# Optimization experiments

Measured on AMD Instinct MI355X. Metric: run time of the kernel, lower is better.

The kernel has to match this reference:

```python
import jax, jax.numpy as jnp
import numpy as np

S, B, D, H = 2048, 2, 1024, 16
DK = D // H


def _rope_tables(seq_len, dk):
    inv_freq = 1.0 / (10000.0 ** (np.arange(0, dk, 2, dtype=np.float32) / dk))
    ang = np.arange(seq_len, dtype=np.float32)[:, None] * inv_freq[None, :]  # [S, dk/2]
    ang = np.concatenate([ang, ang], axis=-1)  # [S, dk]
    cos = jnp.asarray(np.cos(ang))[None, None]  # [1,1,S,dk]
    sin = jnp.asarray(np.sin(ang))[None, None]
    return cos, sin


def rotate_half(x):
    x1, x2 = x[..., : x.shape[-1] // 2], x[..., x.shape[-1] // 2 :]
    return jnp.concatenate([-x2, x1], axis=-1)


def apply_rope(x, cos, sin):
    return x * cos + rotate_half(x) * sin


def setup_inputs() -> dict:
    key = jax.random.key(0)
    ks = jax.random.split(key, 12)
    Q = jax.random.normal(ks[0], (S, B, D), dtype=jnp.float32)
    K = jax.random.normal(ks[1], (S, B, D), dtype=jnp.float32)
    V = jax.random.normal(ks[2], (S, B, D), dtype=jnp.float32)
    s = 0.02
    W_q = jax.random.normal(ks[3], (D, D), dtype=jnp.float32) * s
    W_k = jax.random.normal(ks[4], (D, D), dtype=jnp.float32) * s
    W_v = jax.random.normal(ks[5], (D, D), dtype=jnp.float32) * s
    W_o = jax.random.normal(ks[6], (D, D), dtype=jnp.float32) * s
    b_q = jnp.zeros((D,), jnp.float32)
    b_k = jnp.zeros((D,), jnp.float32)
    b_v = jnp.zeros((D,), jnp.float32)
    b_o = jnp.zeros((D,), jnp.float32)
    cos, sin = _rope_tables(S, DK)
    mask = jnp.triu(jnp.ones((S, S), dtype=bool), k=1)[None, None]  # causal, True = masked
    return {
        "Q": Q, "K": K, "V": V,
        "W_q": W_q, "b_q": b_q, "W_k": W_k, "b_k": b_k,
        "W_v": W_v, "b_v": b_v, "W_o": W_o, "b_o": b_o,
        "q_rotary_cos": cos, "q_rotary_sin": sin,
        "k_rotary_cos": cos, "k_rotary_sin": sin,
        "mask": mask,
    }


def reference(Q, K, V, W_q, b_q, W_k, b_k, W_v, b_v, W_o, b_o,
              q_rotary_cos, q_rotary_sin, k_rotary_cos, k_rotary_sin, mask):
    q_len, bsz, _ = Q.shape
    # [S,B,D] -> [S,B,H,dk] -> [B,H,S,dk]
    def proj(x, W, b):
        y = x @ W.T + b
        return y.reshape(x.shape[0], bsz, H, DK).transpose(1, 2, 0, 3)
    q_s = apply_rope(proj(Q, W_q, b_q), q_rotary_cos, q_rotary_sin)
    k_s = apply_rope(proj(K, W_k, b_k), k_rotary_cos, k_rotary_sin)
    v_s = proj(V, W_v, b_v)
    scores = jnp.einsum("bhqd,bhkd->bhqk", q_s, k_s) / jnp.sqrt(jnp.float32(DK))
    scores = jnp.where(mask, jnp.float32(-1e9), scores)
    attn = jax.nn.softmax(scores, axis=-1)
    context = jnp.einsum("bhqk,bhkd->bhqd", attn, v_s)  # [B,H,S,dk]
    context = context.transpose(2, 0, 1, 3).reshape(q_len, bsz, D)
    return context @ W_o.T + b_o
```

## Files before the change

### kernel.cpp

```cpp
#include <hip/hip_runtime.h>
#include <cstdint>
#include <cstddef>

typedef __bf16 bf16;
typedef __bf16 bf16x2 __attribute__((ext_vector_type(2)));
typedef __bf16 bf16x4 __attribute__((ext_vector_type(4)));
typedef __bf16 bf16x8 __attribute__((ext_vector_type(8)));
typedef float f32x4 __attribute__((ext_vector_type(4)));

#define S_LEN 2048
#define BATCH 2
#define DM 1024
#define NH 16
#define DKH 64
#define MTOT (S_LEN * BATCH)

__device__ __forceinline__ void gload_lds16(const void* g, void* l) {
    __builtin_amdgcn_global_load_lds((const __attribute__((address_space(1))) uint32_t*)g,
                                     (__attribute__((address_space(3))) uint32_t*)l, 16, 0, 0);
}

__device__ __forceinline__ uint32_t pack2(float a, float b) {
    bf16x2 v; v[0] = (bf16)a; v[1] = (bf16)b;
    return __builtin_bit_cast(uint32_t, v);
}

struct ConvArgs { const float* src[7]; bf16* dst[7]; };

__global__ __launch_bounds__(256) void convert_all(ConvArgs a) {
    int gid = blockIdx.x * 256 + threadIdx.x;
    int tid, off;
    if (gid < 3 * 524288) { tid = gid >> 19; off = gid & 524287; }
    else { int r = gid - 3 * 524288; tid = 3 + (r >> 17); off = r & 131071; }
    const float4* s4 = (const float4*)a.src[tid];
    float4 x = s4[2 * off], y = s4[2 * off + 1];
    bf16x8 v;
    v[0] = (bf16)x.x; v[1] = (bf16)x.y; v[2] = (bf16)x.z; v[3] = (bf16)x.w;
    v[4] = (bf16)y.x; v[5] = (bf16)y.y; v[6] = (bf16)y.z; v[7] = (bf16)y.w;
    *(bf16x8*)(a.dst[tid] + 8 * (size_t)off) = v;
}

__device__ __forceinline__ void gemm_core(const bf16* __restrict__ A, const bf16* __restrict__ Bt,
                                          const float* __restrict__ bias, void* __restrict__ out,
                                          int mode, bf16* As, bf16* Bs) {
    const int K = DM;
    int t = threadIdx.x;
    int lane = t & 63, wave = t >> 6;
    int lm = lane & 15, quad = lane >> 4;
    int m0 = blockIdx.y * 128, n0 = blockIdx.x * 128;
    int wm = (wave >> 1) * 64, wn = (wave & 1) * 64;
    f32x4 acc[4][4] = {};
    int g0 = t, g1 = t + 256;
    const bf16* agp0 = A + (size_t)(m0 + (g0 >> 2)) * K + (g0 & 3) * 8;
    const bf16* agp1 = A + (size_t)(m0 + (g1 >> 2)) * K + (g1 & 3) * 8;
    const bf16* bgp0 = Bt + (size_t)(n0 + (g0 >> 2)) * K + (g0 & 3) * 8;
    const bf16* bgp1 = Bt + (size_t)(n0 + (g1 >> 2)) * K + (g1 & 3) * 8;
    bf16* al0 = As + wave * 512;
    bf16* al1 = As + 2048 + wave * 512;
    bf16* bl0 = Bs + wave * 512;
    bf16* bl1 = Bs + 2048 + wave * 512;
    for (int k0 = 0; k0 < K; k0 += 32) {
        gload_lds16(agp0 + k0, al0);
        gload_lds16(agp1 + k0, al1);
        gload_lds16(bgp0 + k0, bl0);
        gload_lds16(bgp1 + k0, bl1);
        __syncthreads();
        bf16x8 af[4], bfr[4];
#pragma unroll
        for (int i = 0; i < 4; ++i)
            af[i] = *(const bf16x8*)(As + (wm + i * 16 + lm) * 32 + quad * 8);
#pragma unroll
        for (int j = 0; j < 4; ++j)
            bfr[j] = *(const bf16x8*)(Bs + (wn + j * 16 + lm) * 32 + quad * 8);
#pragma unroll
        for (int i = 0; i < 4; ++i)
#pragma unroll
            for (int j = 0; j < 4; ++j)
                acc[i][j] = __builtin_amdgcn_mfma_f32_16x16x32_bf16(af[i], bfr[j], acc[i][j], 0, 0, 0);
        __syncthreads();
    }
#pragma unroll
    for (int i = 0; i < 4; ++i) {
#pragma unroll
        for (int j = 0; j < 4; ++j) {
            int col = n0 + wn + j * 16 + lm;
            float bv = bias[col];
            f32x4 v = acc[i][j];
#pragma unroll
            for (int r = 0; r < 4; ++r) {
                int row = m0 + wm + i * 16 + quad * 4 + r;
                float val = v[r] + bv;
                if (mode == 0) {
                    ((bf16*)out)[(size_t)row * DM + col] = (bf16)val;
                } else if (mode == 1) {
                    int s = row >> 1, b = row & 1;
                    int h = col >> 6, dk = col & 63;
                    ((bf16*)out)[((size_t)(b * NH + h) * DKH + dk) * S_LEN + s] = (bf16)val;
                } else {
                    ((float*)out)[(size_t)row * DM + col] = val;
                }
            }
        }
    }
}

struct QKVArgs { const bf16* A[3]; const bf16* W[3]; const float* bias[3]; void* out[3]; int mode[3]; };

__global__ __launch_bounds__(256) void gemm_qkv(QKVArgs args) {
    __shared__ __align__(16) bf16 As[128 * 32];
    __shared__ __align__(16) bf16 Bs[128 * 32];
    int z = blockIdx.z;
    gemm_core(args.A[z], args.W[z], args.bias[z], args.out[z], args.mode[z], As, Bs);
}

__global__ __launch_bounds__(256) void gemm_one(const bf16* __restrict__ A, const bf16* __restrict__ Bt,
                                                const float* __restrict__ bias, void* __restrict__ out,
                                                int mode) {
    __shared__ __align__(16) bf16 As[128 * 32];
    __shared__ __align__(16) bf16 Bs[128 * 32];
    gemm_core(A, Bt, bias, out, mode, As, Bs);
}

__global__ __launch_bounds__(256) void rope_kernel(bf16* __restrict__ q, bf16* __restrict__ k,
                                                   const float* __restrict__ qc, const float* __restrict__ qs,
                                                   const float* __restrict__ kc, const float* __restrict__ ks) {
    int i = blockIdx.x * 256 + threadIdx.x;
    int dk = i & 31;
    int h = (i >> 5) & 15;
    int b = (i >> 9) & 1;
    int s = i >> 10;
    size_t base = ((size_t)s * BATCH + b) * DM + h * DKH;
    int ti = s * DKH + dk;
    const float qscale = 0.125f * 1.44269504088896f;
    float c1 = qc[ti], s1 = qs[ti], c2 = qc[ti + 32], s2 = qs[ti + 32];
    float x1 = (float)q[base + dk], x2 = (float)q[base + dk + 32];
    q[base + dk]      = (bf16)((x1 * c1 - x2 * s1) * qscale);
    q[base + dk + 32] = (bf16)((x2 * c2 + x1 * s2) * qscale);
    float kc1 = kc[ti], ks1 = ks[ti], kc2 = kc[ti + 32], ks2 = ks[ti + 32];
    float y1 = (float)k[base + dk], y2 = (float)k[base + dk + 32];
    k[base + dk]      = (bf16)(y1 * kc1 - y2 * ks1);
    k[base + dk + 32] = (bf16)(y2 * kc2 + y1 * ks2);
}

__global__ __launch_bounds__(256, 2) void flash_kernel(const bf16* __restrict__ qp, const bf16* __restrict__ kp,
                                                       const bf16* __restrict__ vT, bf16* __restrict__ ctx) {
    int qt = 15 - blockIdx.x;
    int bh = blockIdx.y;
    int b = bh >> 4, h = bh & 15;
    int t = threadIdx.x, lane = t & 63, wave = t >> 6;
    int lm = lane & 15, quad = lane >> 4;
    __shared__ __align__(16) bf16 Ks[2 * 64 * 32];
    __shared__ __align__(16) bf16 Vs[2 * 64 * 32];
    __shared__ __align__(16) uint32_t Pb[4][16 * 36];
    uint32_t* pw = &Pb[wave][0];
    const int q0w = qt * 128 + wave * 32;

    bf16x8 aq[2][2];
#pragma unroll
    for (int u = 0; u < 2; ++u) {
        const bf16* qrow = qp + ((size_t)(q0w + u * 16 + lm) * BATCH + b) * DM + h * DKH;
        aq[u][0] = *(const bf16x8*)(qrow + quad * 8);
        aq[u][1] = *(const bf16x8*)(qrow + 32 + quad * 8);
    }
    f32x4 o[2][4] = {};
    float m_u[2] = {-1e30f, -1e30f};
    float l_u[2] = {0.f, 0.f};

    int gA = t, gB = t + 256;
    int aKv = (gA & 255) >> 2, aDq = ((gA >> 8) << 2) + (gA & 3);
    int bKv = (gB & 255) >> 2, bDq = ((gB >> 8) << 2) + (gB & 3);
    const bf16* kgp0 = kp + ((size_t)aKv * BATCH + b) * DM + h * DKH + aDq * 8;
    const bf16* kgp1 = kp + ((size_t)bKv * BATCH + b) * DM + h * DKH + bDq * 8;
    const bf16* vgp0 = vT + ((size_t)bh * DKH + aKv) * S_LEN + aDq * 8;
    const bf16* vgp1 = vT + ((size_t)bh * DKH + bKv) * S_LEN + bDq * 8;
    bf16* kl0 = Ks + wave * 512;
    bf16* kl1 = Ks + 2048 + wave * 512;
    bf16* vl0 = Vs + wave * 512;
    bf16* vl1 = Vs + 2048 + wave * 512;

    const int kv_end = qt * 128 + 128;
    const int wave_qmax = q0w + 31;
    const size_t kstep = (size_t)BATCH * DM;

    for (int kv0 = 0; kv0 < kv_end; kv0 += 64) {
        gload_lds16(kgp0 + (size_t)kv0 * kstep, kl0);
        gload_lds16(kgp1 + (size_t)kv0 * kstep, kl1);
        gload_lds16(vgp0 + kv0, vl0);
        gload_lds16(vgp1 + kv0, vl1);
        __syncthreads();
        if (kv0 <= wave_qmax) {
            bf16x8 kf[4][2], vf[4][2];
#pragma unroll
            for (int nt = 0; nt < 4; ++nt) {
                kf[nt][0] = *(const bf16x8*)(Ks + (nt * 16 + lm) * 32 + quad * 8);
                kf[nt][1] = *(const bf16x8*)(Ks + 2048 + (nt * 16 + lm) * 32 + quad * 8);
            }
#pragma unroll
            for (int dt = 0; dt < 4; ++dt) {
                vf[dt][0] = *(const bf16x8*)(Vs + (dt * 16 + lm) * 32 + quad * 8);
                vf[dt][1] = *(const bf16x8*)(Vs + 2048 + (dt * 16 + lm) * 32 + quad * 8);
            }
            const f32x4 zero = {0.f, 0.f, 0.f, 0.f};
            f32x4 sc[2][4];
#pragma unroll
            for (int u = 0; u < 2; ++u)
#pragma unroll
                for (int nt = 0; nt < 4; ++nt) {
                    sc[u][nt] = __builtin_amdgcn_mfma_f32_16x16x32_bf16(kf[nt][0], aq[u][0], zero, 0, 0, 0);
                    sc[u][nt] = __builtin_amdgcn_mfma_f32_16x16x32_bf16(kf[nt][1], aq[u][1], sc[u][nt], 0, 0, 0);
                }
#pragma unroll
            for (int u = 0; u < 2; ++u) {
                int qu0 = q0w + u * 16;
                if (kv0 + 63 > qu0) {
#pragma unroll
                    for (int nt = 0; nt < 4; ++nt)
#pragma unroll
                        for (int r = 0; r < 4; ++r) {
                            int kvg = kv0 + nt * 16 + quad * 4 + r;
                            if (kvg > qu0 + lm) sc[u][nt][r] = -1e30f;
                        }
                }
            }
#pragma unroll
            for (int u = 0; u < 2; ++u) {
                float mx = sc[u][0][0];
#pragma unroll
                for (int nt = 0; nt < 4; ++nt)
#pragma unroll
                    for (int r = 0; r < 4; ++r) mx = fmaxf(mx, sc[u][nt][r]);
                mx = fmaxf(mx, __shfl_xor(mx, 16, 64));
                mx = fmaxf(mx, __shfl_xor(mx, 32, 64));
                float mn = fmaxf(m_u[u], mx);
                float al = exp2f(m_u[u] - mn);
                m_u[u] = mn;
                float rs = 0.f;
                uint32_t pk[8];
#pragma unroll
                for (int nt = 0; nt < 4; ++nt)
#pragma unroll
                    for (int rp = 0; rp < 2; ++rp) {
                        float p0 = exp2f(sc[u][nt][2 * rp] - mn);
                        float p1 = exp2f(sc[u][nt][2 * rp + 1] - mn);
                        rs += p0 + p1;
                        pk[nt * 2 + rp] = pack2(p0, p1);
                    }
                rs += __shfl_xor(rs, 16, 64);
                rs += __shfl_xor(rs, 32, 64);
                l_u[u] = l_u[u] * al + rs;
#pragma unroll
                for (int dt = 0; dt < 4; ++dt) o[u][dt] *= al;
#pragma unroll
                for (int nt = 0; nt < 4; ++nt)
#pragma unroll
                    for (int rp = 0; rp < 2; ++rp)
                        pw[lm * 36 + nt * 8 + quad * 2 + rp] = pk[nt * 2 + rp];
                __builtin_amdgcn_wave_barrier();
                const uint32_t* pr = pw + lm * 36;
                bf16x8 pf0 = *(const bf16x8*)(pr + quad * 4);
                bf16x8 pf1 = *(const bf16x8*)(pr + 16 + quad * 4);
#pragma unroll
                for (int dt = 0; dt < 4; ++dt) {
                    o[u][dt] = __builtin_amdgcn_mfma_f32_16x16x32_bf16(vf[dt][0], pf0, o[u][dt], 0, 0, 0);
                    o[u][dt] = __builtin_amdgcn_mfma_f32_16x16x32_bf16(vf[dt][1], pf1, o[u][dt], 0, 0, 0);
                }
                __builtin_amdgcn_wave_barrier();
            }
        }
        __syncthreads();
    }
#pragma unroll
    for (int u = 0; u < 2; ++u) {
        float linv = 1.f / l_u[u];
        int qg = q0w + u * 16 + lm;
        bf16* crow = ctx + ((size_t)qg * BATCH + b) * DM + h * DKH;
#pragma unroll
        for (int dt = 0; dt < 4; ++dt) {
            bf16x4 v;
#pragma unroll
            for (int r = 0; r < 4; ++r) v[r] = (bf16)(o[u][dt][r] * linv);
            *(bf16x4*)(crow + dt * 16 + quad * 4) = v;
        }
    }
}

extern "C" void kernel_launch(void* const* d_in, const int* in_sizes, int n_in,
                              void* d_out, int out_size, void* d_ws, size_t ws_size,
                              hipStream_t stream) {
    const float* Q    = (const float*)d_in[0];
    const float* K    = (const float*)d_in[1];
    const float* V    = (const float*)d_in[2];
    const float* Wq   = (const float*)d_in[3];
    const float* bq   = (const float*)d_in[4];
    const float* Wk   = (const float*)d_in[5];
    const float* bk   = (const float*)d_in[6];
    const float* Wv   = (const float*)d_in[7];
    const float* bv   = (const float*)d_in[8];
    const float* Wo   = (const float*)d_in[9];
    const float* bo   = (const float*)d_in[10];
    const float* qcos = (const float*)d_in[11];
    const float* qsin = (const float*)d_in[12];
    const float* kcos = (const float*)d_in[13];
    const float* ksin = (const float*)d_in[14];

    char* ws = (char*)d_ws;
    const size_t SZ_ACT = (size_t)MTOT * DM * sizeof(bf16);
    const size_t SZ_W   = (size_t)DM * DM * sizeof(bf16);
    bf16* qb  = (bf16*)ws; ws += SZ_ACT;
    bf16* kb  = (bf16*)ws; ws += SZ_ACT;
    bf16* vb  = (bf16*)ws; ws += SZ_ACT;
    bf16* wqb = (bf16*)ws; ws += SZ_W;
    bf16* wkb = (bf16*)ws; ws += SZ_W;
    bf16* wvb = (bf16*)ws; ws += SZ_W;
    bf16* wob = (bf16*)ws; ws += SZ_W;
    bf16* qpr = (bf16*)ws; ws += SZ_ACT;
    bf16* kpr = (bf16*)ws; ws += SZ_ACT;
    bf16* vTp = (bf16*)ws; ws += SZ_ACT;
    bf16* ctx = (bf16*)ws; ws += SZ_ACT;

    ConvArgs ca;
    ca.src[0] = Q;  ca.dst[0] = qb;
    ca.src[1] = K;  ca.dst[1] = kb;
    ca.src[2] = V;  ca.dst[2] = vb;
    ca.src[3] = Wq; ca.dst[3] = wqb;
    ca.src[4] = Wk; ca.dst[4] = wkb;
    ca.src[5] = Wv; ca.dst[5] = wvb;
    ca.src[6] = Wo; ca.dst[6] = wob;
    convert_all<<<8192, 256, 0, stream>>>(ca);

    QKVArgs qa;
    qa.A[0] = qb; qa.W[0] = wqb; qa.bias[0] = bq; qa.out[0] = qpr; qa.mode[0] = 0;
    qa.A[1] = kb; qa.W[1] = wkb; qa.bias[1] = bk; qa.out[1] = kpr; qa.mode[1] = 0;
    qa.A[2] = vb; qa.W[2] = wvb; qa.bias[2] = bv; qa.out[2] = vTp; qa.mode[2] = 1;
    gemm_qkv<<<dim3(DM / 128, MTOT / 128, 3), 256, 0, stream>>>(qa);

    rope_kernel<<<(S_LEN * BATCH * NH * 32) / 256, 256, 0, stream>>>(qpr, kpr, qcos, qsin, kcos, ksin);

    flash_kernel<<<dim3(S_LEN / 128, BATCH * NH), 256, 0, stream>>>(qpr, kpr, vTp, ctx);

    gemm_one<<<dim3(DM / 128, MTOT / 128), 256, 0, stream>>>(ctx, wob, bo, (float*)d_out, 2);
}
```

Baseline: 301.4 us.

## Fuse RoPE into QKV GEMM epilogue and restructure flash attention tiling

Applies the rotary embedding and the softmax scale inside the Q/K projection GEMM epilogue. It pairs each column with its partner accumulator (j^2, a 32-column offset within the 64-wide head), which removes the separate rope kernel and its extra read/write pass. The flash kernel changes to 64-query tiles with one 16-row strip per wave, 32 blocks per head and launch bounds of 3. K/V staging changes from direct global-to-LDS loads to register-prefetched double buffering with padded LDS rows (72 elements). This trades more grid parallelism and overlap for less reuse of each K/V tile across query rows.

```diff
diff --git a/kernel.cpp b/kernel.cpp
--- a/kernel.cpp
+++ b/kernel.cpp
@@ -42,7 +42,8 @@
 
 __device__ __forceinline__ void gemm_core(const bf16* __restrict__ A, const bf16* __restrict__ Bt,
                                           const float* __restrict__ bias, void* __restrict__ out,
-                                          int mode, bf16* As, bf16* Bs) {
+                                          int mode, const float* __restrict__ cosp,
+                                          const float* __restrict__ sinp, bf16* As, bf16* Bs) {
     const int K = DM;
     int t = threadIdx.x;
     int lane = t & 63, wave = t >> 6;
@@ -80,207 +81,202 @@
         __syncthreads();
     }
 #pragma unroll
+    for (int j = 0; j < 4; ++j) {
+        float bcol = bias[n0 + wn + j * 16 + lm];
+#pragma unroll
+        for (int i = 0; i < 4; ++i)
+#pragma unroll
+            for (int r = 0; r < 4; ++r) acc[i][j][r] += bcol;
+    }
+#pragma unroll
     for (int i = 0; i < 4; ++i) {
 #pragma unroll
         for (int j = 0; j < 4; ++j) {
             int col = n0 + wn + j * 16 + lm;
-            float bv = bias[col];
-            f32x4 v = acc[i][j];
 #pragma unroll
             for (int r = 0; r < 4; ++r) {
                 int row = m0 + wm + i * 16 + quad * 4 + r;
-                float val = v[r] + bv;
-                if (mode == 0) {
-                    ((bf16*)out)[(size_t)row * DM + col] = (bf16)val;
-                } else if (mode == 1) {
+                float val = acc[i][j][r];
+                if (mode == 1) {
                     int s = row >> 1, b = row & 1;
                     int h = col >> 6, dk = col & 63;
                     ((bf16*)out)[((size_t)(b * NH + h) * DKH + dk) * S_LEN + s] = (bf16)val;
+                } else if (mode == 2) {
+                    ((float*)out)[(size_t)row * DM + col] = val;
                 } else {
-                    ((float*)out)[(size_t)row * DM + col] = val;
+                    int s = row >> 1, dk = col & 63;
+                    float c = cosp[s * 64 + dk], sn = sinp[s * 64 + dk];
+                    float partner = acc[i][j ^ 2][r];
+                    float v2 = val * c + (dk < 32 ? -partner : partner) * sn;
+                    if (mode == 3) v2 *= 0.125f * 1.44269504088896f;
+                    ((bf16*)out)[(size_t)row * DM + col] = (bf16)v2;
                 }
             }
         }
     }
 }
 
-struct QKVArgs { const bf16* A[3]; const bf16* W[3]; const float* bias[3]; void* out[3]; int mode[3]; };
+struct QKVArgs {
+    const bf16* A[3]; const bf16* W[3]; const float* bias[3];
+    void* out[3]; const float* cs[3]; const float* sn[3]; int mode[3];
+};
 
 __global__ __launch_bounds__(256) void gemm_qkv(QKVArgs args) {
     __shared__ __align__(16) bf16 As[128 * 32];
     __shared__ __align__(16) bf16 Bs[128 * 32];
     int z = blockIdx.z;
-    gemm_core(args.A[z], args.W[z], args.bias[z], args.out[z], args.mode[z], As, Bs);
+    gemm_core(args.A[z], args.W[z], args.bias[z], args.out[z], args.mode[z],
+              args.cs[z], args.sn[z], As, Bs);
 }
 
 __global__ __launch_bounds__(256) void gemm_one(const bf16* __restrict__ A, const bf16* __restrict__ Bt,
-                                                const float* __restrict__ bias, void* __restrict__ out,
-                                                int mode) {
+                                                const float* __restrict__ bias, void* __restrict__ out) {
     __shared__ __align__(16) bf16 As[128 * 32];
     __shared__ __align__(16) bf16 Bs[128 * 32];
-    gemm_core(A, Bt, bias, out, mode, As, Bs);
-}
-
-__global__ __launch_bounds__(256) void rope_kernel(bf16* __restrict__ q, bf16* __restrict__ k,
-                                                   const float* __restrict__ qc, const float* __restrict__ qs,
-                                                   const float* __restrict__ kc, const float* __restrict__ ks) {
-    int i = blockIdx.x * 256 + threadIdx.x;
-    int dk = i & 31;
-    int h = (i >> 5) & 15;
-    int b = (i >> 9) & 1;
-    int s = i >> 10;
-    size_t base = ((size_t)s * BATCH + b) * DM + h * DKH;
-    int ti = s * DKH + dk;
-    const float qscale = 0.125f * 1.44269504088896f;
-    float c1 = qc[ti], s1 = qs[ti], c2 = qc[ti + 32], s2 = qs[ti + 32];
-    float x1 = (float)q[base + dk], x2 = (float)q[base + dk + 32];
-    q[base + dk]      = (bf16)((x1 * c1 - x2 * s1) * qscale);
-    q[base + dk + 32] = (bf16)((x2 * c2 + x1 * s2) * qscale);
-    float kc1 = kc[ti], ks1 = ks[ti], kc2 = kc[ti + 32], ks2 = ks[ti + 32];
-    float y1 = (float)k[base + dk], y2 = (float)k[base + dk + 32];
-    k[base + dk]      = (bf16)(y1 * kc1 - y2 * ks1);
-    k[base + dk + 32] = (bf16)(y2 * kc2 + y1 * ks2);
-}
-
-__global__ __launch_bounds__(256, 2) void flash_kernel(const bf16* __restrict__ qp, const bf16* __restrict__ kp,
+    gemm_core(A, Bt, bias, out, 2, nullptr, nullptr, As, Bs);
+}
+
+#define LROW 72
+#define LBUF (64 * LROW)
+
+__global__ __launch_bounds__(256, 3) void flash_kernel(const bf16* __restrict__ qp, const bf16* __restrict__ kp,
                                                        const bf16* __restrict__ vT, bf16* __restrict__ ctx) {
-    int qt = 15 - blockIdx.x;
+    int qt = 31 - blockIdx.x;
     int bh = blockIdx.y;
     int b = bh >> 4, h = bh & 15;
     int t = threadIdx.x, lane = t & 63, wave = t >> 6;
     int lm = lane & 15, quad = lane >> 4;
-    __shared__ __align__(16) bf16 Ks[2 * 64 * 32];
-    __shared__ __align__(16) bf16 Vs[2 * 64 * 32];
+    __shared__ __align__(16) bf16 Ks[2 * LBUF];
+    __shared__ __align__(16) bf16 Vs[2 * LBUF];
     __shared__ __align__(16) uint32_t Pb[4][16 * 36];
     uint32_t* pw = &Pb[wave][0];
-    const int q0w = qt * 128 + wave * 32;
-
-    bf16x8 aq[2][2];
-#pragma unroll
-    for (int u = 0; u < 2; ++u) {
-        const bf16* qrow = qp + ((size_t)(q0w + u * 16 + lm) * BATCH + b) * DM + h * DKH;
-        aq[u][0] = *(const bf16x8*)(qrow + quad * 8);
-        aq[u][1] = *(const bf16x8*)(qrow + 32 + quad * 8);
-    }
-    f32x4 o[2][4] = {};
-    float m_u[2] = {-1e30f, -1e30f};
-    float l_u[2] = {0.f, 0.f};
-
-    int gA = t, gB = t + 256;
-    int aKv = (gA & 255) >> 2, aDq = ((gA >> 8) << 2) + (gA & 3);
-    int bKv = (gB & 255) >> 2, bDq = ((gB >> 8) << 2) + (gB & 3);
-    const bf16* kgp0 = kp + ((size_t)aKv * BATCH + b) * DM + h * DKH + aDq * 8;
-    const bf16* kgp1 = kp + ((size_t)bKv * BATCH + b) * DM + h * DKH + bDq * 8;
-    const bf16* vgp0 = vT + ((size_t)bh * DKH + aKv) * S_LEN + aDq * 8;
-    const bf16* vgp1 = vT + ((size_t)bh * DKH + bKv) * S_LEN + bDq * 8;
-    bf16* kl0 = Ks + wave * 512;
-    bf16* kl1 = Ks + 2048 + wave * 512;
-    bf16* vl0 = Vs + wave * 512;
-    bf16* vl1 = Vs + 2048 + wave * 512;
-
-    const int kv_end = qt * 128 + 128;
-    const int wave_qmax = q0w + 31;
+    const int q0w = qt * 64 + wave * 16;
     const size_t kstep = (size_t)BATCH * DM;
 
-    for (int kv0 = 0; kv0 < kv_end; kv0 += 64) {
-        gload_lds16(kgp0 + (size_t)kv0 * kstep, kl0);
-        gload_lds16(kgp1 + (size_t)kv0 * kstep, kl1);
-        gload_lds16(vgp0 + kv0, vl0);
-        gload_lds16(vgp1 + kv0, vl1);
-        __syncthreads();
-        if (kv0 <= wave_qmax) {
-            bf16x8 kf[4][2], vf[4][2];
+    const bf16* qrow = qp + ((size_t)(q0w + lm) * BATCH + b) * DM + h * DKH;
+    bf16x8 aq0 = *(const bf16x8*)(qrow + quad * 8);
+    bf16x8 aq1 = *(const bf16x8*)(qrow + 32 + quad * 8);
+    f32x4 o[4] = {};
+    float m_i = -1e30f, l_i = 0.f;
+
+    int g0 = t, g1 = t + 256;
+    int r0 = g0 >> 3, c0 = g0 & 7, r1 = g1 >> 3, c1 = g1 & 7;
+    const bf16* kg0 = kp + ((size_t)r0 * BATCH + b) * DM + h * DKH + c0 * 8;
+    const bf16* kg1 = kp + ((size_t)r1 * BATCH + b) * DM + h * DKH + c1 * 8;
+    const bf16* vg0 = vT + ((size_t)(bh * DKH + r0)) * S_LEN + c0 * 8;
+    const bf16* vg1 = vT + ((size_t)(bh * DKH + r1)) * S_LEN + c1 * 8;
+    int lo0 = r0 * LROW + c0 * 8;
+    int lo1 = r1 * LROW + c1 * 8;
+
+    const int niter = qt + 1;
+    {
+        bf16x8 ka = *(const bf16x8*)kg0;
+        bf16x8 kb2 = *(const bf16x8*)kg1;
+        bf16x8 va = *(const bf16x8*)vg0;
+        bf16x8 vb2 = *(const bf16x8*)vg1;
+        *(bf16x8*)(Ks + lo0) = ka;
+        *(bf16x8*)(Ks + lo1) = kb2;
+        *(bf16x8*)(Vs + lo0) = va;
+        *(bf16x8*)(Vs + lo1) = vb2;
+    }
+    __syncthreads();
+
+    for (int it = 0; it < niter; ++it) {
+        int kv0 = it << 6;
+        int cb = it & 1, nb = cb ^ 1;
+        bool hn = (it + 1) < niter;
+        bf16x8 ka, kb2, va, vb2;
+        if (hn) {
+            size_t koff = (size_t)(kv0 + 64) * kstep;
+            ka  = *(const bf16x8*)(kg0 + koff);
+            kb2 = *(const bf16x8*)(kg1 + koff);
+            va  = *(const bf16x8*)(vg0 + kv0 + 64);
+            vb2 = *(const bf16x8*)(vg1 + kv0 + 64);
+        }
+        if (kv0 <= q0w + 15) {
+            const bf16* Kb = Ks + cb * LBUF;
+            const bf16* Vb = Vs + cb * LBUF;
+            const f32x4 zero = {0.f, 0.f, 0.f, 0.f};
+            f32x4 sc[4];
 #pragma unroll
             for (int nt = 0; nt < 4; ++nt) {
-                kf[nt][0] = *(const bf16x8*)(Ks + (nt * 16 + lm) * 32 + quad * 8);
-                kf[nt][1] = *(const bf16x8*)(Ks + 2048 + (nt * 16 + lm) * 32 + quad * 8);
+                bf16x8 kf0 = *(const bf16x8*)(Kb + (nt * 16 + lm) * LROW + quad * 8);
+                bf16x8 kf1 = *(const bf16x8*)(Kb + (nt * 16 + lm) * LROW + 32 + quad * 8);
+                sc[nt] = __builtin_amdgcn_mfma_f32_16x16x32_bf16(kf0, aq0, zero, 0, 0, 0);
+                sc[nt] = __builtin_amdgcn_mfma_f32_16x16x32_bf16(kf1, aq1, sc[nt], 0, 0, 0);
             }
+            if (kv0 + 63 > q0w) {
+#pragma unroll
+                for (int nt = 0; nt < 4; ++nt)
+#pragma unroll
+                    for (int r = 0; r < 4; ++r) {
+                        int kvg = kv0 + nt * 16 + quad * 4 + r;
+                        if (kvg > q0w + lm) sc[nt][r] = -1e30f;
+                    }
+            }
+            float mx = sc[0][0];
+#pragma unroll
+            for (int nt = 0; nt < 4; ++nt)
+#pragma unroll
+                for (int r = 0; r < 4; ++r) mx = fmaxf(mx, sc[nt][r]);
+            mx = fmaxf(mx, __shfl_xor(mx, 16, 64));
+            mx = fmaxf(mx, __shfl_xor(mx, 32, 64));
+            float mn = fmaxf(m_i, mx);
+            float al = exp2f(m_i - mn);
+            m_i = mn;
+            float rs = 0.f;
+            uint32_t pk[8];
+#pragma unroll
+            for (int nt = 0; nt < 4; ++nt)
+#pragma unroll
+                for (int rp = 0; rp < 2; ++rp) {
+                    float p0 = exp2f(sc[nt][2 * rp] - mn);
+                    float p1 = exp2f(sc[nt][2 * rp + 1] - mn);
+                    rs += p0 + p1;
+                    pk[nt * 2 + rp] = pack2(p0, p1);
+                }
+            rs += __shfl_xor(rs, 16, 64);
+            rs += __shfl_xor(rs, 32, 64);
+            l_i = l_i * al + rs;
+#pragma unroll
+            for (int dt = 0; dt < 4; ++dt) o[dt] *= al;
+#pragma unroll
+            for (int nt = 0; nt < 4; ++nt)
+#pragma unroll
+                for (int rp = 0; rp < 2; ++rp)
+                    pw[lm * 36 + nt * 8 + quad * 2 + rp] = pk[nt * 2 + rp];
+            __builtin_amdgcn_wave_barrier();
+            const uint32_t* pr = pw + lm * 36;
+            bf16x8 pf0 = *(const bf16x8*)(pr + quad * 4);
+            bf16x8 pf1 = *(const bf16x8*)(pr + 16 + quad * 4);
 #pragma unroll
             for (int dt = 0; dt < 4; ++dt) {
-                vf[dt][0] = *(const bf16x8*)(Vs + (dt * 16 + lm) * 32 + quad * 8);
-                vf[dt][1] = *(const bf16x8*)(Vs + 2048 + (dt * 16 + lm) * 32 + quad * 8);
+                bf16x8 vf0 = *(const bf16x8*)(Vb + (dt * 16 + lm) * LROW + quad * 8);
+                bf16x8 vf1 = *(const bf16x8*)(Vb + (dt * 16 + lm) * LROW + 32 + quad * 8);
+                o[dt] = __builtin_amdgcn_mfma_f32_16x16x32_bf16(vf0, pf0, o[dt], 0, 0, 0);
+                o[dt] = __builtin_amdgcn_mfma_f32_16x16x32_bf16(vf1, pf1, o[dt], 0, 0, 0);
             }
-            const f32x4 zero = {0.f, 0.f, 0.f, 0.f};
-            f32x4 sc[2][4];
-#pragma unroll
-            for (int u = 0; u < 2; ++u)
-#pragma unroll
-                for (int nt = 0; nt < 4; ++nt) {
-                    sc[u][nt] = __builtin_amdgcn_mfma_f32_16x16x32_bf16(kf[nt][0], aq[u][0], zero, 0, 0, 0);
-                    sc[u][nt] = __builtin_amdgcn_mfma_f32_16x16x32_bf16(kf[nt][1], aq[u][1], sc[u][nt], 0, 0, 0);
-                }
-#pragma unroll
-            for (int u = 0; u < 2; ++u) {
-                int qu0 = q0w + u * 16;
-                if (kv0 + 63 > qu0) {
-#pragma unroll
-                    for (int nt = 0; nt < 4; ++nt)
-#pragma unroll
-                        for (int r = 0; r < 4; ++r) {
-                            int kvg = kv0 + nt * 16 + quad * 4 + r;
-                            if (kvg > qu0 + lm) sc[u][nt][r] = -1e30f;
-                        }
-                }
-            }
-#pragma unroll
-            for (int u = 0; u < 2; ++u) {
-                float mx = sc[u][0][0];
-#pragma unroll
-                for (int nt = 0; nt < 4; ++nt)
-#pragma unroll
-                    for (int r = 0; r < 4; ++r) mx = fmaxf(mx, sc[u][nt][r]);
-                mx = fmaxf(mx, __shfl_xor(mx, 16, 64));
-                mx = fmaxf(mx, __shfl_xor(mx, 32, 64));
-                float mn = fmaxf(m_u[u], mx);
-                float al = exp2f(m_u[u] - mn);
-                m_u[u] = mn;
-                float rs = 0.f;
-                uint32_t pk[8];
-#pragma unroll
-                for (int nt = 0; nt < 4; ++nt)
-#pragma unroll
-                    for (int rp = 0; rp < 2; ++rp) {
-                        float p0 = exp2f(sc[u][nt][2 * rp] - mn);
-                        float p1 = exp2f(sc[u][nt][2 * rp + 1] - mn);
-                        rs += p0 + p1;
-                        pk[nt * 2 + rp] = pack2(p0, p1);
-                    }
-                rs += __shfl_xor(rs, 16, 64);
-                rs += __shfl_xor(rs, 32, 64);
-                l_u[u] = l_u[u] * al + rs;
-#pragma unroll
-                for (int dt = 0; dt < 4; ++dt) o[u][dt] *= al;
-#pragma unroll
-                for (int nt = 0; nt < 4; ++nt)
-#pragma unroll
-                    for (int rp = 0; rp < 2; ++rp)
-                        pw[lm * 36 + nt * 8 + quad * 2 + rp] = pk[nt * 2 + rp];
-                __builtin_amdgcn_wave_barrier();
-                const uint32_t* pr = pw + lm * 36;
-                bf16x8 pf0 = *(const bf16x8*)(pr + quad * 4);
-                bf16x8 pf1 = *(const bf16x8*)(pr + 16 + quad * 4);
-#pragma unroll
-                for (int dt = 0; dt < 4; ++dt) {
-                    o[u][dt] = __builtin_amdgcn_mfma_f32_16x16x32_bf16(vf[dt][0], pf0, o[u][dt], 0, 0, 0);
-                    o[u][dt] = __builtin_amdgcn_mfma_f32_16x16x32_bf16(vf[dt][1], pf1, o[u][dt], 0, 0, 0);
-                }
-                __builtin_amdgcn_wave_barrier();
-            }
+            __builtin_amdgcn_wave_barrier();
+        }
+        if (hn) {
+            bf16* Kn = Ks + nb * LBUF;
+            bf16* Vn = Vs + nb * LBUF;
+            *(bf16x8*)(Kn + lo0) = ka;
+            *(bf16x8*)(Kn + lo1) = kb2;
+            *(bf16x8*)(Vn + lo0) = va;
+            *(bf16x8*)(Vn + lo1) = vb2;
         }
         __syncthreads();
     }
-#pragma unroll
-    for (int u = 0; u < 2; ++u) {
-        float linv = 1.f / l_u[u];
-        int qg = q0w + u * 16 + lm;
-        bf16* crow = ctx + ((size_t)qg * BATCH + b) * DM + h * DKH;
-#pragma unroll
-        for (int dt = 0; dt < 4; ++dt) {
-            bf16x4 v;
-#pragma unroll
-            for (int r = 0; r < 4; ++r) v[r] = (bf16)(o[u][dt][r] * linv);
-            *(bf16x4*)(crow + dt * 16 + quad * 4) = v;
-        }
+    float linv = 1.f / l_i;
+    int qg = q0w + lm;
+    bf16* crow = ctx + ((size_t)qg * BATCH + b) * DM + h * DKH;
+#pragma unroll
+    for (int dt = 0; dt < 4; ++dt) {
+        bf16x4 v;
+#pragma unroll
+        for (int r = 0; r < 4; ++r) v[r] = (bf16)(o[dt][r] * linv);
+        *(bf16x4*)(crow + dt * 16 + quad * 4) = v;
     }
 }
 
@@ -329,14 +325,12 @@
     convert_all<<<8192, 256, 0, stream>>>(ca);
 
     QKVArgs qa;
-    qa.A[0] = qb; qa.W[0] = wqb; qa.bias[0] = bq; qa.out[0] = qpr; qa.mode[0] = 0;
-    qa.A[1] = kb; qa.W[1] = wkb; qa.bias[1] = bk; qa.out[1] = kpr; qa.mode[1] = 0;
-    qa.A[2] = vb; qa.W[2] = wvb; qa.bias[2] = bv; qa.out[2] = vTp; qa.mode[2] = 1;
+    qa.A[0] = qb; qa.W[0] = wqb; qa.bias[0] = bq; qa.out[0] = qpr; qa.mode[0] = 3; qa.cs[0] = qcos; qa.sn[0] = qsin;
+    qa.A[1] = kb; qa.W[1] = wkb; qa.bias[1] = bk; qa.out[1] = kpr; qa.mode[1] = 4; qa.cs[1] = kcos; qa.sn[1] = ksin;
+    qa.A[2] = vb; qa.W[2] = wvb; qa.bias[2] = bv; qa.out[2] = vTp; qa.mode[2] = 1; qa.cs[2] = nullptr; qa.sn[2] = nullptr;
     gemm_qkv<<<dim3(DM / 128, MTOT / 128, 3), 256, 0, stream>>>(qa);
 
-    rope_kernel<<<(S_LEN * BATCH * NH * 32) / 256, 256, 0, stream>>>(qpr, kpr, qcos, qsin, kcos, ksin);
-
-    flash_kernel<<<dim3(S_LEN / 128, BATCH * NH), 256, 0, stream>>>(qpr, kpr, vTp, ctx);
-
-    gemm_one<<<dim3(DM / 128, MTOT / 128), 256, 0, stream>>>(ctx, wob, bo, (float*)d_out, 2);
-}
+    flash_kernel<<<dim3(32, BATCH * NH), 256, 0, stream>>>(qpr, kpr, vTp, ctx);
+
+    gemm_one<<<dim3(DM / 128, MTOT / 128), 256, 0, stream>>>(ctx, wob, bo, (float*)d_out);
+}
```

Result: slower. 309.9 us (+2.8%).
